# Kernel optimization log

Measured on AMD Instinct MI355X. Metric: run time of the kernel, lower is better.

## Reference

```python
import jax, jax.numpy as jnp
import numpy as np

N, DEG, D, L = 20000, 32, 128, 2
EPS = 1e-7
MAX_TANH_ARG = 1.0 - 1e-5


def _logmap0(x, sqrt_c):
    # Poincare ball log map at the origin: artanh(sqrt(c)||x||) * x / (sqrt(c)||x||)
    norm = jnp.maximum(jnp.linalg.norm(x, axis=-1, keepdims=True), EPS)
    arg = jnp.minimum(sqrt_c * norm, MAX_TANH_ARG)
    return jnp.arctanh(arg) * x / (sqrt_c * norm)


def _expmap0(v, sqrt_c):
    # Poincare ball exp map at the origin: tanh(sqrt(c)||v||) * v / (sqrt(c)||v||)
    norm = jnp.maximum(jnp.linalg.norm(v, axis=-1, keepdims=True), EPS)
    return jnp.tanh(sqrt_c * norm) * v / (sqrt_c * norm)


def setup_inputs() -> dict:
    key = jax.random.key(0)
    ks = jax.random.split(key, 7)
    neighbors = jax.random.randint(ks[0], (N, DEG), 0, N)  # fixed in-degree predecessor lists
    node_embeddings = jax.random.normal(ks[1], (N, D), dtype=jnp.float32)
    in_proj_w = jax.random.normal(ks[2], (L, 3 * D, D), dtype=jnp.float32) * 0.02
    in_proj_b = jax.random.normal(ks[3], (L, 3 * D), dtype=jnp.float32) * 0.02
    out_proj_w = jax.random.normal(ks[4], (L, D, D), dtype=jnp.float32) * 0.02
    out_proj_b = jax.random.normal(ks[5], (L, D), dtype=jnp.float32) * 0.02
    curvature = jnp.array([-1.0], dtype=jnp.float32)
    return {
        'neighbors': neighbors,
        'node_embeddings': node_embeddings,
        'curvature': curvature,
        'in_proj_w': in_proj_w,
        'in_proj_b': in_proj_b,
        'out_proj_w': out_proj_w,
        'out_proj_b': out_proj_b,
    }


def reference(neighbors, node_embeddings, curvature, in_proj_w, in_proj_b, out_proj_w, out_proj_b):
    sqrt_c = jnp.sqrt(jnp.abs(curvature[0]))
    scale = 1.0 / np.sqrt(D)  # torch MHA scales q by 1/sqrt(head_dim)
    x = node_embeddings
    for l in range(L):
        t = _logmap0(x, sqrt_c)                       # [N, d] tangent features
        Wq, Wk, Wv = in_proj_w[l, :D], in_proj_w[l, D:2 * D], in_proj_w[l, 2 * D:]
        bq, bk, bv = in_proj_b[l, :D], in_proj_b[l, D:2 * D], in_proj_b[l, 2 * D:]
        q = t @ Wq.T + bq                             # [N, d]
        k = t @ Wk.T + bk
        v = t @ Wv.T + bv
        kn = k[neighbors]                             # [N, deg, d] gather over predecessors
        vn = v[neighbors]                             # [N, deg, d]
        scores = jnp.einsum('nd,nkd->nk', q, kn) * scale
        attn = jax.nn.softmax(scores, axis=-1)        # [N, deg]
        h = jnp.einsum('nk,nkd->nd', attn, vn)        # [N, d]
        h = h @ out_proj_w[l].T + out_proj_b[l]
        x = _expmap0(h, sqrt_c)
    return x
```

## Files before the change

### kernel.cpp

```cpp
#include <hip/hip_runtime.h>

#define N_NODES 20000
#define N_PAD   20032
#define DEG 32
#define D 128
#define EPS 1e-7f
#define MAX_TANH_ARG (1.0f - 1e-5f)
#define SCORE_SCALE 0.08838834764831845f

typedef short bf16x8 __attribute__((ext_vector_type(8)));
typedef float f32x4 __attribute__((ext_vector_type(4)));

__device__ __forceinline__ float b2f(unsigned short u) {
  union { unsigned int i; float f; } x; x.i = ((unsigned int)u) << 16; return x.f;
}
__device__ __forceinline__ unsigned short f2b(float f) {
  union { float f; unsigned int i; } x; x.f = f;
  unsigned int r = x.i + 0x7FFFu + ((x.i >> 16) & 1u);
  return (unsigned short)(r >> 16);
}
__device__ __forceinline__ bool inputs_are_bf16(const void* curv) {
  return *(const unsigned short*)curv != 0;
}
__device__ __forceinline__ float read_sqrt_c(const void* c) {
  unsigned short u = *(const unsigned short*)c;
  float cv = (u == 0) ? *(const float*)c : b2f(u);
  return sqrtf(fabsf(cv));
}
__device__ __forceinline__ float atanh_fast(float x) {
  return 0.5f * __logf((1.f + x) / (1.f - x));
}
__device__ __forceinline__ float tanh_over_y(float y) {
  float e = __expf(-2.f * y);
  return (1.f - e) / ((1.f + e) * y);
}

__device__ __forceinline__ unsigned char f2fp8(float v) {
#if __has_builtin(__builtin_amdgcn_cvt_pk_fp8_f32)
  int p = __builtin_amdgcn_cvt_pk_fp8_f32(v, 0.f, 0, false);
  return (unsigned char)(p & 0xFF);
#else
  union { float f; unsigned u; } x; x.f = v;
  unsigned s = (x.u >> 31) << 7;
  float a = fminf(fabsf(v), 448.f);
  int q = (int)rintf(a * 512.f);
  if (q < 8) return (unsigned char)(s | q);
  int e; float m = frexpf(a, &e);
  int E = e - 1 + 7;
  int mi = (int)rintf(m * 16.f) - 8;
  if (mi == 8) { mi = 0; E += 1; }
  if (E > 15) { E = 15; mi = 6; }
  if (E < 1)  { return (unsigned char)(s | ((int)rintf(a * 512.f) & 7)); }
  return (unsigned char)(s | (E << 3) | mi);
#endif
}
__device__ __forceinline__ void fp8x8_decode(uint2 w, float* f) {
#if __has_builtin(__builtin_amdgcn_cvt_f32_fp8)
  f[0] = __builtin_amdgcn_cvt_f32_fp8((int)w.x, 0);
  f[1] = __builtin_amdgcn_cvt_f32_fp8((int)w.x, 1);
  f[2] = __builtin_amdgcn_cvt_f32_fp8((int)w.x, 2);
  f[3] = __builtin_amdgcn_cvt_f32_fp8((int)w.x, 3);
  f[4] = __builtin_amdgcn_cvt_f32_fp8((int)w.y, 0);
  f[5] = __builtin_amdgcn_cvt_f32_fp8((int)w.y, 1);
  f[6] = __builtin_amdgcn_cvt_f32_fp8((int)w.y, 2);
  f[7] = __builtin_amdgcn_cvt_f32_fp8((int)w.y, 3);
#else
#pragma unroll
  for (int i = 0; i < 8; i++) {
    unsigned char u = (i < 4) ? (unsigned char)(w.x >> (8 * i))
                              : (unsigned char)(w.y >> (8 * (i - 4)));
    int e = (u >> 3) & 15, m = u & 7;
    float mag = e ? ldexpf((float)(8 + m), e - 10) : ldexpf((float)m, -9);
    f[i] = (u & 0x80) ? -mag : mag;
  }
#endif
}

__global__ __launch_bounds__(256) void convert_kernel(
    const void* __restrict__ s0, unsigned short* __restrict__ d0, int n0,
    const void* __restrict__ s1, unsigned short* __restrict__ d1, int n1,
    const void* __restrict__ s2, unsigned short* __restrict__ d2, int n2,
    const void* __restrict__ s3, unsigned short* __restrict__ d3, int n3,
    const void* __restrict__ curv) {
  bool bf = inputs_are_bf16(curv);
  int total = n0 + n1 + n2 + n3;
  for (int i = blockIdx.x * 256 + threadIdx.x; i < total; i += gridDim.x * 256) {
    int idx = i;
    const void* s; unsigned short* d;
    if (idx < n0)                { s = s0; d = d0; }
    else if ((idx -= n0) < n1)   { s = s1; d = d1; }
    else if ((idx -= n1) < n2)   { s = s2; d = d2; }
    else { idx -= n2;              s = s3; d = d3; }
    d[idx] = bf ? ((const unsigned short*)s)[idx]
                : f2b(((const float*)s)[idx]);
  }
}

__device__ __forceinline__ void qkv_store(
    int m0, int quad, int l16, int nbase, bool isq,
    const f32x4* acc,
    const unsigned short* bias, unsigned short* qout, unsigned char* out8) {
#pragma unroll
  for (int half = 0; half < 2; half++) {
#pragma unroll
    for (int s = 0; s < 4; s++) {
      int ncol = half * 64 + s * 16 + l16;
      float bv = b2f(bias[nbase + ncol]);
#pragma unroll
      for (int r = 0; r < 4; r++) {
        int m = m0 + quad * 4 + r;
        if (m < N_NODES) {
          float val = acc[half * 4 + s][r] + bv;
          if (isq) qout[(size_t)m * D + ncol] = f2b(val);
          else     out8[(size_t)m * D + ncol] = f2fp8(val);
        }
      }
    }
  }
}

__device__ __forceinline__ void qkv_mfma(
    const bf16x8* a, const unsigned short* W, int nbase, int quad, int l16,
    f32x4* acc) {
#pragma unroll
  for (int half = 0; half < 2; half++) {
    int n0g = nbase + half * 64;
#pragma unroll
    for (int s = 0; s < 4; s++) {
      acc[half * 4 + s] = {0.f, 0.f, 0.f, 0.f};
      const short* brow = (const short*)W + (size_t)(n0g + s * 16 + l16) * D + quad * 8;
#pragma unroll
      for (int kk = 0; kk < 4; kk++) {
        bf16x8 bfv = *(const bf16x8*)(brow + kk * 32);
        acc[half * 4 + s] = __builtin_amdgcn_mfma_f32_16x16x32_bf16(a[kk], bfv, acc[half * 4 + s], 0, 0, 0);
      }
    }
  }
}

__global__ __launch_bounds__(256) void lqkv_kernel(
    const void* __restrict__ xin,
    const unsigned short* __restrict__ W,
    const unsigned short* __restrict__ bias,
    unsigned short* __restrict__ qout,
    unsigned char* __restrict__ kout,
    unsigned char* __restrict__ vout,
    const void* __restrict__ curv) {
  __shared__ unsigned short t_lds[64 * 136];
  int lane = threadIdx.x & 63;
  int wave = threadIdx.x >> 6;
  int mbase = blockIdx.x * 64;
  bool srcbf = inputs_are_bf16(curv);
  float sqc = read_sqrt_c(curv);

  {
    int rl = threadIdx.x >> 3;
    int c8 = threadIdx.x & 7;
#pragma unroll
    for (int pass = 0; pass < 2; pass++) {
      int r = pass * 32 + rl;
      int m = mbase + r;
      float xv[16];
      if (m < N_NODES) {
        if (srcbf) {
          const bf16x8* xp = (const bf16x8*)((const unsigned short*)xin + (size_t)m * D + c8 * 16);
          bf16x8 u0 = xp[0], u1 = xp[1];
#pragma unroll
          for (int i = 0; i < 8; i++) { xv[i] = b2f((unsigned short)u0[i]); xv[8 + i] = b2f((unsigned short)u1[i]); }
        } else {
          const float4* xp = (const float4*)((const float*)xin + (size_t)m * D + c8 * 16);
#pragma unroll
          for (int i = 0; i < 4; i++) {
            float4 v = xp[i];
            xv[i * 4 + 0] = v.x; xv[i * 4 + 1] = v.y; xv[i * 4 + 2] = v.z; xv[i * 4 + 3] = v.w;
          }
        }
      } else {
#pragma unroll
        for (int i = 0; i < 16; i++) xv[i] = 0.f;
      }
      float ss = 0.f;
#pragma unroll
      for (int i = 0; i < 16; i++) ss += xv[i] * xv[i];
      ss += __shfl_xor(ss, 1); ss += __shfl_xor(ss, 2); ss += __shfl_xor(ss, 4);
      float norm = fmaxf(sqrtf(ss), EPS);
      float arg  = fminf(sqc * norm, MAX_TANH_ARG);
      float sfac = atanh_fast(arg) / (sqc * norm);
      bf16x8 o0, o1;
#pragma unroll
      for (int i = 0; i < 8; i++) {
        o0[i] = (short)f2b(xv[i] * sfac);
        o1[i] = (short)f2b(xv[8 + i] * sfac);
      }
      *(bf16x8*)&t_lds[r * 136 + c8 * 16]     = o0;
      *(bf16x8*)&t_lds[r * 136 + c8 * 16 + 8] = o1;
    }
  }
  __syncthreads();

  int quad = lane >> 4, l16 = lane & 15;
  int m0 = mbase + wave * 16;
  bf16x8 a[4];
#pragma unroll
  for (int kk = 0; kk < 4; kk++)
    a[kk] = *(const bf16x8*)&t_lds[(wave * 16 + l16) * 136 + quad * 8 + kk * 32];

  int nbase = blockIdx.y * 128;
  f32x4 acc[8];
  qkv_mfma(a, W, nbase, quad, l16, acc);
  qkv_store(m0, quad, l16, nbase, blockIdx.y == 0, acc, bias,
            qout, (blockIdx.y == 1) ? kout : vout);
}

__global__ __launch_bounds__(256) void qkv_direct_kernel(
    const unsigned short* __restrict__ t,
    const unsigned short* __restrict__ W,
    const unsigned short* __restrict__ bias,
    unsigned short* __restrict__ qout,
    unsigned char* __restrict__ kout,
    unsigned char* __restrict__ vout) {
  int lane = threadIdx.x & 63;
  int wave = threadIdx.x >> 6;
  int quad = lane >> 4, l16 = lane & 15;
  int m0 = blockIdx.x * 64 + wave * 16;

  bf16x8 a[4];
  const short* arow = (const short*)t + (size_t)(m0 + l16) * D + quad * 8;
#pragma unroll
  for (int kk = 0; kk < 4; kk++) a[kk] = *(const bf16x8*)(arow + kk * 32);

  int nbase = blockIdx.y * 128;
  f32x4 acc[8];
  qkv_mfma(a, W, nbase, quad, l16, acc);
  qkv_store(m0, quad, l16, nbase, blockIdx.y == 0, acc, bias,
            qout, (blockIdx.y == 1) ? kout : vout);
}

__global__ __launch_bounds__(256) void attn_kernel(
    const int* __restrict__ nbrs,
    const unsigned short* __restrict__ qb,
    const unsigned char* __restrict__ k8,
    const unsigned char* __restrict__ v8,
    unsigned short* __restrict__ hout) {
  int gid  = blockIdx.x * 256 + threadIdx.x;
  int node = gid >> 6;
  int lane = gid & 63;
  if (node >= N_NODES) return;
  int g = lane >> 4;
  int s = lane & 15;

  float qr[8];
  {
    bf16x8 qv = *(const bf16x8*)(qb + (size_t)node * D + s * 8);
#pragma unroll
    for (int i = 0; i < 8; i++) qr[i] = b2f((unsigned short)qv[i]);
  }
  int idx[8];
#pragma unroll
  for (int jj = 0; jj < 8; jj++) idx[jj] = nbrs[node * DEG + jj * 4 + g];

  uint2 kreg[8], vreg[8];
#pragma unroll
  for (int jj = 0; jj < 8; jj++)
    kreg[jj] = *(const uint2*)(k8 + (size_t)idx[jj] * D + s * 8);
#pragma unroll
  for (int jj = 0; jj < 8; jj++)
    vreg[jj] = *(const uint2*)(v8 + (size_t)idx[jj] * D + s * 8);

  float sc[8];
#pragma unroll
  for (int jj = 0; jj < 8; jj++) {
    float kf[8];
    fp8x8_decode(kreg[jj], kf);
    float p = 0.f;
#pragma unroll
    for (int i = 0; i < 8; i++) p += kf[i] * qr[i];
    p += __shfl_xor(p, 1); p += __shfl_xor(p, 2);
    p += __shfl_xor(p, 4); p += __shfl_xor(p, 8);
    sc[jj] = p * SCORE_SCALE;
  }

  float mx = sc[0];
#pragma unroll
  for (int jj = 1; jj < 8; jj++) mx = fmaxf(mx, sc[jj]);
  mx = fmaxf(mx, __shfl_xor(mx, 16));
  mx = fmaxf(mx, __shfl_xor(mx, 32));
  float sum = 0.f;
#pragma unroll
  for (int jj = 0; jj < 8; jj++) { sc[jj] = __expf(sc[jj] - mx); sum += sc[jj]; }
  sum += __shfl_xor(sum, 16);
  sum += __shfl_xor(sum, 32);
  float inv = 1.f / sum;

  float hv[8];
#pragma unroll
  for (int i = 0; i < 8; i++) hv[i] = 0.f;
#pragma unroll
  for (int jj = 0; jj < 8; jj++) {
    float aw = sc[jj] * inv;
    float vf[8];
    fp8x8_decode(vreg[jj], vf);
#pragma unroll
    for (int i = 0; i < 8; i++) hv[i] += aw * vf[i];
  }
#pragma unroll
  for (int i = 0; i < 8; i++) {
    hv[i] += __shfl_xor(hv[i], 16);
    hv[i] += __shfl_xor(hv[i], 32);
  }
  if (g == 0) {
    bf16x8 o;
#pragma unroll
    for (int i = 0; i < 8; i++) o[i] = (short)f2b(hv[i]);
    *(bf16x8*)(hout + (size_t)node * D + s * 8) = o;
  }
}

template <int MODE>
__global__ __launch_bounds__(256) void outproj_kernel(
    const short* __restrict__ h,
    const unsigned short* __restrict__ W,
    const unsigned short* __restrict__ bias,
    void* __restrict__ xout,
    const void* __restrict__ curv) {
  int wave = threadIdx.x >> 6;
  int lane = threadIdx.x & 63;
  int quad = lane >> 4;
  int l16  = lane & 15;
  int m0   = blockIdx.x * 64 + wave * 16;

  bf16x8 a[4];
  const short* arow = h + (size_t)(m0 + l16) * D + quad * 8;
#pragma unroll
  for (int kk = 0; kk < 4; kk++) a[kk] = *(const bf16x8*)(arow + kk * 32);

  f32x4 acc[8];
#pragma unroll
  for (int s = 0; s < 8; s++) acc[s] = {0.f, 0.f, 0.f, 0.f};
#pragma unroll
  for (int s = 0; s < 8; s++) {
    const short* brow = (const short*)W + (size_t)(s * 16 + l16) * D + quad * 8;
#pragma unroll
    for (int kk = 0; kk < 4; kk++) {
      bf16x8 bfv = *(const bf16x8*)(brow + kk * 32);
      acc[s] = __builtin_amdgcn_mfma_f32_16x16x32_bf16(a[kk], bfv, acc[s], 0, 0, 0);
    }
  }
#pragma unroll
  for (int s = 0; s < 8; s++) {
    float bv = b2f(bias[s * 16 + l16]);
#pragma unroll
    for (int r = 0; r < 4; r++) acc[s][r] += bv;
  }
  float scal[4];
  if (MODE == 1) {
    float sqc = read_sqrt_c(curv);
#pragma unroll
    for (int r = 0; r < 4; r++) {
      float ss = 0.f;
#pragma unroll
      for (int s = 0; s < 8; s++) ss += acc[s][r] * acc[s][r];
      ss += __shfl_xor(ss, 1); ss += __shfl_xor(ss, 2);
      ss += __shfl_xor(ss, 4); ss += __shfl_xor(ss, 8);
      float norm = fmaxf(sqrtf(ss), EPS);
      scal[r] = tanh_over_y(sqc * norm);
    }
  }
  bool outbf = (MODE == 1) && inputs_are_bf16(curv);
#pragma unroll
  for (int r = 0; r < 4; r++) {
    int m = m0 + quad * 4 + r;
    if (m < N_NODES) {
#pragma unroll
      for (int s = 0; s < 8; s++) {
        int col = s * 16 + l16;
        if (MODE == 0) {
          ((unsigned short*)xout)[(size_t)m * D + col] = f2b(acc[s][r]);
        } else {
          float val = acc[s][r] * scal[r];
          if (outbf) ((unsigned short*)xout)[(size_t)m * D + col] = f2b(val);
          else       ((float*)xout)[(size_t)m * D + col] = val;
        }
      }
    }
  }
}

extern "C" void kernel_launch(void* const* d_in, const int* in_sizes, int n_in,
                              void* d_out, int out_size, void* d_ws, size_t ws_size,
                              hipStream_t stream) {
  const int* neighbors = (const int*)d_in[0];
  const void* node_emb = d_in[1];
  const void* curv     = d_in[2];
  const void* in_w     = d_in[3];
  const void* in_b     = d_in[4];
  const void* out_w    = d_in[5];
  const void* out_b    = d_in[6];

  char* ws = (char*)d_ws;
  size_t off = 0;
  auto alloc = [&](size_t bytes) {
    char* p = ws + off; off += (bytes + 255) & ~(size_t)255; return p;
  };
  unsigned short* q_bf = (unsigned short*)alloc((size_t)N_PAD * D * 2);
  unsigned char*  k_f8 = (unsigned char*)alloc((size_t)N_PAD * D);
  unsigned char*  v_f8 = (unsigned char*)alloc((size_t)N_PAD * D);
  unsigned short* h_bf = (unsigned short*)alloc((size_t)N_PAD * D * 2);
  unsigned short* t1_bf = (unsigned short*)alloc((size_t)N_PAD * D * 2);
  const int n_inw = 2 * 384 * D, n_inb = 2 * 384, n_outw = 2 * D * D, n_outb = 2 * D;
  unsigned short* inw_bf  = (unsigned short*)alloc((size_t)n_inw * 2);
  unsigned short* inb_bf  = (unsigned short*)alloc((size_t)n_inb * 2);
  unsigned short* outw_bf = (unsigned short*)alloc((size_t)n_outw * 2);
  unsigned short* outb_bf = (unsigned short*)alloc((size_t)n_outb * 2);

  dim3 blk(256);
  int nodeBlocks = (N_NODES + 3) / 4;
  int mTiles     = (N_NODES + 63) / 64;

  convert_kernel<<<208, blk, 0, stream>>>(
      in_w, inw_bf, n_inw, in_b, inb_bf, n_inb,
      out_w, outw_bf, n_outw, out_b, outb_bf, n_outb, curv);

  lqkv_kernel<<<dim3(mTiles, 3), blk, 0, stream>>>(
      node_emb, inw_bf, inb_bf, q_bf, k_f8, v_f8, curv);
  attn_kernel<<<nodeBlocks, blk, 0, stream>>>(neighbors, q_bf, k_f8, v_f8, h_bf);
  outproj_kernel<0><<<mTiles, blk, 0, stream>>>(
      (const short*)h_bf, outw_bf, outb_bf, t1_bf, curv);

  qkv_direct_kernel<<<dim3(mTiles, 3), blk, 0, stream>>>(
      t1_bf, inw_bf + (size_t)384 * D, inb_bf + 384, q_bf, k_f8, v_f8);
  attn_kernel<<<nodeBlocks, blk, 0, stream>>>(neighbors, q_bf, k_f8, v_f8, h_bf);
  outproj_kernel<1><<<mTiles, blk, 0, stream>>>(
      (const short*)h_bf, outw_bf + (size_t)D * D, outb_bf + D, d_out, curv);
}
```

Before: 184.5 us.

## Drop weight conversion kernel and fuse layer-0 out-proj with layer-1 QKV

Removes the separate weight-to-bf16 conversion kernel; GEMM kernels now load fp32 or bf16 weights directly and convert in registers. The layer-0 output projection and layer-1 QKV projection are fused into one kernel that stages the projected tile in LDS, which avoids a global round trip of the intermediate t1 and one launch. The cost is that each block converts fp32 weights on the fly for every tile, and the fused kernel runs only 313 blocks that each do three QKV phases serially, so there is less parallelism.

```diff
diff --git a/kernel.cpp b/kernel.cpp
--- a/kernel.cpp
+++ b/kernel.cpp
@@ -7,6 +7,7 @@
 #define EPS 1e-7f
 #define MAX_TANH_ARG (1.0f - 1e-5f)
 #define SCORE_SCALE 0.08838834764831845f
+#define MTILES 313
 
 typedef short bf16x8 __attribute__((ext_vector_type(8)));
 typedef float f32x4 __attribute__((ext_vector_type(4)));
@@ -33,6 +34,21 @@
 __device__ __forceinline__ float tanh_over_y(float y) {
   float e = __expf(-2.f * y);
   return (1.f - e) / ((1.f + e) * y);
+}
+
+__device__ __forceinline__ bf16x8 load8(const void* p, size_t off, bool bf) {
+  if (bf) return *(const bf16x8*)((const unsigned short*)p + off);
+  const float4* q4 = (const float4*)((const float*)p + off);
+  float4 a = q4[0], b = q4[1];
+  bf16x8 o;
+  o[0] = (short)f2b(a.x); o[1] = (short)f2b(a.y);
+  o[2] = (short)f2b(a.z); o[3] = (short)f2b(a.w);
+  o[4] = (short)f2b(b.x); o[5] = (short)f2b(b.y);
+  o[6] = (short)f2b(b.z); o[7] = (short)f2b(b.w);
+  return o;
+}
+__device__ __forceinline__ float load1(const void* p, size_t off, bool bf) {
+  return bf ? b2f(((const unsigned short*)p)[off]) : ((const float*)p)[off];
 }
 
 __device__ __forceinline__ unsigned char f2fp8(float v) {
@@ -76,36 +92,32 @@
 #endif
 }
 
-__global__ __launch_bounds__(256) void convert_kernel(
-    const void* __restrict__ s0, unsigned short* __restrict__ d0, int n0,
-    const void* __restrict__ s1, unsigned short* __restrict__ d1, int n1,
-    const void* __restrict__ s2, unsigned short* __restrict__ d2, int n2,
-    const void* __restrict__ s3, unsigned short* __restrict__ d3, int n3,
-    const void* __restrict__ curv) {
-  bool bf = inputs_are_bf16(curv);
-  int total = n0 + n1 + n2 + n3;
-  for (int i = blockIdx.x * 256 + threadIdx.x; i < total; i += gridDim.x * 256) {
-    int idx = i;
-    const void* s; unsigned short* d;
-    if (idx < n0)                { s = s0; d = d0; }
-    else if ((idx -= n0) < n1)   { s = s1; d = d1; }
-    else if ((idx -= n1) < n2)   { s = s2; d = d2; }
-    else { idx -= n2;              s = s3; d = d3; }
-    d[idx] = bf ? ((const unsigned short*)s)[idx]
-                : f2b(((const float*)s)[idx]);
-  }
-}
-
-__device__ __forceinline__ void qkv_store(
-    int m0, int quad, int l16, int nbase, bool isq,
-    const f32x4* acc,
-    const unsigned short* bias, unsigned short* qout, unsigned char* out8) {
+__device__ __forceinline__ void qkv_phase(
+    const bf16x8* a, const void* W, size_t woff, const void* bias, size_t boff,
+    bool srcbf, int m0, int quad, int l16, int nbase,
+    unsigned short* qout, unsigned char* out8, bool isq) {
+  f32x4 acc[8];
+#pragma unroll
+  for (int half = 0; half < 2; half++) {
+    int n0g = nbase + half * 64;
+#pragma unroll
+    for (int s = 0; s < 4; s++) {
+      f32x4 c = {0.f, 0.f, 0.f, 0.f};
+      size_t base = woff + (size_t)(n0g + s * 16 + l16) * D + quad * 8;
+#pragma unroll
+      for (int kk = 0; kk < 4; kk++) {
+        bf16x8 bfv = load8(W, base + kk * 32, srcbf);
+        c = __builtin_amdgcn_mfma_f32_16x16x32_bf16(a[kk], bfv, c, 0, 0, 0);
+      }
+      acc[half * 4 + s] = c;
+    }
+  }
 #pragma unroll
   for (int half = 0; half < 2; half++) {
 #pragma unroll
     for (int s = 0; s < 4; s++) {
       int ncol = half * 64 + s * 16 + l16;
-      float bv = b2f(bias[nbase + ncol]);
+      float bv = load1(bias, boff + nbase + ncol, srcbf);
 #pragma unroll
       for (int r = 0; r < 4; r++) {
         int m = m0 + quad * 4 + r;
@@ -119,32 +131,31 @@
   }
 }
 
-__device__ __forceinline__ void qkv_mfma(
-    const bf16x8* a, const unsigned short* W, int nbase, int quad, int l16,
-    f32x4* acc) {
-#pragma unroll
-  for (int half = 0; half < 2; half++) {
-    int n0g = nbase + half * 64;
-#pragma unroll
-    for (int s = 0; s < 4; s++) {
-      acc[half * 4 + s] = {0.f, 0.f, 0.f, 0.f};
-      const short* brow = (const short*)W + (size_t)(n0g + s * 16 + l16) * D + quad * 8;
-#pragma unroll
-      for (int kk = 0; kk < 4; kk++) {
-        bf16x8 bfv = *(const bf16x8*)(brow + kk * 32);
-        acc[half * 4 + s] = __builtin_amdgcn_mfma_f32_16x16x32_bf16(a[kk], bfv, acc[half * 4 + s], 0, 0, 0);
-      }
-    }
+__device__ __forceinline__ void outproj_acc(
+    const unsigned short* __restrict__ h, const void* W, size_t woff,
+    bool srcbf, int m0, int quad, int l16, f32x4* acc) {
+  bf16x8 a[4];
+  const short* arow = (const short*)h + (size_t)(m0 + l16) * D + quad * 8;
+#pragma unroll
+  for (int kk = 0; kk < 4; kk++) a[kk] = *(const bf16x8*)(arow + kk * 32);
+#pragma unroll
+  for (int s = 0; s < 8; s++) {
+    f32x4 c = {0.f, 0.f, 0.f, 0.f};
+    size_t base = woff + (size_t)(s * 16 + l16) * D + quad * 8;
+#pragma unroll
+    for (int kk = 0; kk < 4; kk++) {
+      bf16x8 bfv = load8(W, base + kk * 32, srcbf);
+      c = __builtin_amdgcn_mfma_f32_16x16x32_bf16(a[kk], bfv, c, 0, 0, 0);
+    }
+    acc[s] = c;
   }
 }
 
 __global__ __launch_bounds__(256) void lqkv_kernel(
     const void* __restrict__ xin,
-    const unsigned short* __restrict__ W,
-    const unsigned short* __restrict__ bias,
+    const void* __restrict__ in_w, const void* __restrict__ in_b,
     unsigned short* __restrict__ qout,
-    unsigned char* __restrict__ kout,
-    unsigned char* __restrict__ vout,
+    unsigned char* __restrict__ kout, unsigned char* __restrict__ vout,
     const void* __restrict__ curv) {
   __shared__ unsigned short t_lds[64 * 136];
   int lane = threadIdx.x & 63;
@@ -199,41 +210,14 @@
   __syncthreads();
 
   int quad = lane >> 4, l16 = lane & 15;
-  int m0 = mbase + wave * 16;
   bf16x8 a[4];
 #pragma unroll
   for (int kk = 0; kk < 4; kk++)
     a[kk] = *(const bf16x8*)&t_lds[(wave * 16 + l16) * 136 + quad * 8 + kk * 32];
 
-  int nbase = blockIdx.y * 128;
-  f32x4 acc[8];
-  qkv_mfma(a, W, nbase, quad, l16, acc);
-  qkv_store(m0, quad, l16, nbase, blockIdx.y == 0, acc, bias,
-            qout, (blockIdx.y == 1) ? kout : vout);
-}
-
-__global__ __launch_bounds__(256) void qkv_direct_kernel(
-    const unsigned short* __restrict__ t,
-    const unsigned short* __restrict__ W,
-    const unsigned short* __restrict__ bias,
-    unsigned short* __restrict__ qout,
-    unsigned char* __restrict__ kout,
-    unsigned char* __restrict__ vout) {
-  int lane = threadIdx.x & 63;
-  int wave = threadIdx.x >> 6;
-  int quad = lane >> 4, l16 = lane & 15;
-  int m0 = blockIdx.x * 64 + wave * 16;
-
-  bf16x8 a[4];
-  const short* arow = (const short*)t + (size_t)(m0 + l16) * D + quad * 8;
-#pragma unroll
-  for (int kk = 0; kk < 4; kk++) a[kk] = *(const bf16x8*)(arow + kk * 32);
-
-  int nbase = blockIdx.y * 128;
-  f32x4 acc[8];
-  qkv_mfma(a, W, nbase, quad, l16, acc);
-  qkv_store(m0, quad, l16, nbase, blockIdx.y == 0, acc, bias,
-            qout, (blockIdx.y == 1) ? kout : vout);
+  int y = blockIdx.y;
+  qkv_phase(a, in_w, 0, in_b, 0, srcbf, mbase + wave * 16, quad, l16, y * 128,
+            qout, (y == 1) ? kout : vout, y == 0);
 }
 
 __global__ __launch_bounds__(256) void attn_kernel(
@@ -279,7 +263,6 @@
     p += __shfl_xor(p, 4); p += __shfl_xor(p, 8);
     sc[jj] = p * SCORE_SCALE;
   }
-
   float mx = sc[0];
 #pragma unroll
   for (int jj = 1; jj < 8; jj++) mx = fmaxf(mx, sc[jj]);
@@ -316,71 +299,86 @@
   }
 }
 
-template <int MODE>
-__global__ __launch_bounds__(256) void outproj_kernel(
-    const short* __restrict__ h,
-    const unsigned short* __restrict__ W,
-    const unsigned short* __restrict__ bias,
-    void* __restrict__ xout,
+__global__ __launch_bounds__(256) void op_qkv_kernel(
+    const unsigned short* __restrict__ h,
+    const void* __restrict__ out_w, const void* __restrict__ out_b,
+    const void* __restrict__ in_w, const void* __restrict__ in_b,
+    unsigned short* __restrict__ qout,
+    unsigned char* __restrict__ kout, unsigned char* __restrict__ vout,
     const void* __restrict__ curv) {
+  __shared__ unsigned short t_lds[64 * 136];
+  int lane = threadIdx.x & 63;
   int wave = threadIdx.x >> 6;
+  int quad = lane >> 4, l16 = lane & 15;
+  int m0 = blockIdx.x * 64 + wave * 16;
+  bool srcbf = inputs_are_bf16(curv);
+
+  {
+    f32x4 acc[8];
+    outproj_acc(h, out_w, 0, srcbf, m0, quad, l16, acc);
+#pragma unroll
+    for (int s = 0; s < 8; s++) {
+      float bv = load1(out_b, s * 16 + l16, srcbf);
+#pragma unroll
+      for (int r = 0; r < 4; r++) {
+        int rloc = wave * 16 + quad * 4 + r;
+        t_lds[rloc * 136 + s * 16 + l16] = f2b(acc[s][r] + bv);
+      }
+    }
+  }
+  __syncthreads();
+
+  bf16x8 a[4];
+#pragma unroll
+  for (int kk = 0; kk < 4; kk++)
+    a[kk] = *(const bf16x8*)&t_lds[(wave * 16 + l16) * 136 + quad * 8 + kk * 32];
+#pragma unroll
+  for (int y = 0; y < 3; y++) {
+    qkv_phase(a, in_w, (size_t)384 * D, in_b, 384, srcbf,
+              m0, quad, l16, y * 128, qout, (y == 1) ? kout : vout, y == 0);
+  }
+}
+
+__global__ __launch_bounds__(256) void outproj_final_kernel(
+    const unsigned short* __restrict__ h,
+    const void* __restrict__ out_w, const void* __restrict__ out_b,
+    void* __restrict__ xout, const void* __restrict__ curv) {
   int lane = threadIdx.x & 63;
-  int quad = lane >> 4;
-  int l16  = lane & 15;
-  int m0   = blockIdx.x * 64 + wave * 16;
-
-  bf16x8 a[4];
-  const short* arow = h + (size_t)(m0 + l16) * D + quad * 8;
-#pragma unroll
-  for (int kk = 0; kk < 4; kk++) a[kk] = *(const bf16x8*)(arow + kk * 32);
+  int wave = threadIdx.x >> 6;
+  int quad = lane >> 4, l16 = lane & 15;
+  int m0 = blockIdx.x * 64 + wave * 16;
+  bool srcbf = inputs_are_bf16(curv);
+  float sqc = read_sqrt_c(curv);
 
   f32x4 acc[8];
-#pragma unroll
-  for (int s = 0; s < 8; s++) acc[s] = {0.f, 0.f, 0.f, 0.f};
+  outproj_acc(h, out_w, (size_t)D * D, srcbf, m0, quad, l16, acc);
 #pragma unroll
   for (int s = 0; s < 8; s++) {
-    const short* brow = (const short*)W + (size_t)(s * 16 + l16) * D + quad * 8;
-#pragma unroll
-    for (int kk = 0; kk < 4; kk++) {
-      bf16x8 bfv = *(const bf16x8*)(brow + kk * 32);
-      acc[s] = __builtin_amdgcn_mfma_f32_16x16x32_bf16(a[kk], bfv, acc[s], 0, 0, 0);
-    }
-  }
-#pragma unroll
-  for (int s = 0; s < 8; s++) {
-    float bv = b2f(bias[s * 16 + l16]);
+    float bv = load1(out_b, D + s * 16 + l16, srcbf);
 #pragma unroll
     for (int r = 0; r < 4; r++) acc[s][r] += bv;
   }
   float scal[4];
-  if (MODE == 1) {
-    float sqc = read_sqrt_c(curv);
-#pragma unroll
-    for (int r = 0; r < 4; r++) {
-      float ss = 0.f;
-#pragma unroll
-      for (int s = 0; s < 8; s++) ss += acc[s][r] * acc[s][r];
-      ss += __shfl_xor(ss, 1); ss += __shfl_xor(ss, 2);
-      ss += __shfl_xor(ss, 4); ss += __shfl_xor(ss, 8);
-      float norm = fmaxf(sqrtf(ss), EPS);
-      scal[r] = tanh_over_y(sqc * norm);
-    }
-  }
-  bool outbf = (MODE == 1) && inputs_are_bf16(curv);
+#pragma unroll
+  for (int r = 0; r < 4; r++) {
+    float ss = 0.f;
+#pragma unroll
+    for (int s = 0; s < 8; s++) ss += acc[s][r] * acc[s][r];
+    ss += __shfl_xor(ss, 1); ss += __shfl_xor(ss, 2);
+    ss += __shfl_xor(ss, 4); ss += __shfl_xor(ss, 8);
+    float norm = fmaxf(sqrtf(ss), EPS);
+    scal[r] = tanh_over_y(sqc * norm);
+  }
 #pragma unroll
   for (int r = 0; r < 4; r++) {
     int m = m0 + quad * 4 + r;
     if (m < N_NODES) {
 #pragma unroll
       for (int s = 0; s < 8; s++) {
+        float val = acc[s][r] * scal[r];
         int col = s * 16 + l16;
-        if (MODE == 0) {
-          ((unsigned short*)xout)[(size_t)m * D + col] = f2b(acc[s][r]);
-        } else {
-          float val = acc[s][r] * scal[r];
-          if (outbf) ((unsigned short*)xout)[(size_t)m * D + col] = f2b(val);
-          else       ((float*)xout)[(size_t)m * D + col] = val;
-        }
+        if (srcbf) ((unsigned short*)xout)[(size_t)m * D + col] = f2b(val);
+        else       ((float*)xout)[(size_t)m * D + col] = val;
       }
     }
   }
@@ -406,30 +404,15 @@
   unsigned char*  k_f8 = (unsigned char*)alloc((size_t)N_PAD * D);
   unsigned char*  v_f8 = (unsigned char*)alloc((size_t)N_PAD * D);
   unsigned short* h_bf = (unsigned short*)alloc((size_t)N_PAD * D * 2);
-  unsigned short* t1_bf = (unsigned short*)alloc((size_t)N_PAD * D * 2);
-  const int n_inw = 2 * 384 * D, n_inb = 2 * 384, n_outw = 2 * D * D, n_outb = 2 * D;
-  unsigned short* inw_bf  = (unsigned short*)alloc((size_t)n_inw * 2);
-  unsigned short* inb_bf  = (unsigned short*)alloc((size_t)n_inb * 2);
-  unsigned short* outw_bf = (unsigned short*)alloc((size_t)n_outw * 2);
-  unsigned short* outb_bf = (unsigned short*)alloc((size_t)n_outb * 2);
 
   dim3 blk(256);
-  int nodeBlocks = (N_NODES + 3) / 4;
-  int mTiles     = (N_NODES + 63) / 64;
-
-  convert_kernel<<<208, blk, 0, stream>>>(
-      in_w, inw_bf, n_inw, in_b, inb_bf, n_inb,
-      out_w, outw_bf, n_outw, out_b, outb_bf, n_outb, curv);
-
-  lqkv_kernel<<<dim3(mTiles, 3), blk, 0, stream>>>(
-      node_emb, inw_bf, inb_bf, q_bf, k_f8, v_f8, curv);
-  attn_kernel<<<nodeBlocks, blk, 0, stream>>>(neighbors, q_bf, k_f8, v_f8, h_bf);
-  outproj_kernel<0><<<mTiles, blk, 0, stream>>>(
-      (const short*)h_bf, outw_bf, outb_bf, t1_bf, curv);
-
-  qkv_direct_kernel<<<dim3(mTiles, 3), blk, 0, stream>>>(
-      t1_bf, inw_bf + (size_t)384 * D, inb_bf + 384, q_bf, k_f8, v_f8);
-  attn_kernel<<<nodeBlocks, blk, 0, stream>>>(neighbors, q_bf, k_f8, v_f8, h_bf);
-  outproj_kernel<1><<<mTiles, blk, 0, stream>>>(
-      (const short*)h_bf, outw_bf + (size_t)D * D, outb_bf + D, d_out, curv);
-}
+
+  lqkv_kernel<<<dim3(MTILES, 3), blk, 0, stream>>>(
+      node_emb, in_w, in_b, q_bf, k_f8, v_f8, curv);
+  attn_kernel<<<5000, blk, 0, stream>>>(neighbors, q_bf, k_f8, v_f8, h_bf);
+  op_qkv_kernel<<<MTILES, blk, 0, stream>>>(
+      h_bf, out_w, out_b, in_w, in_b, q_bf, k_f8, v_f8, curv);
+  attn_kernel<<<5000, blk, 0, stream>>>(neighbors, q_bf, k_f8, v_f8, h_bf);
+  outproj_final_kernel<<<MTILES, blk, 0, stream>>>(
+      h_bf, out_w, out_b, d_out, curv);
+}
```

After: 272.3 us. +47.6%, slower.
